# Performance work log

Measured on AMD Instinct MI355X. Metric: run time of the kernel, lower is better.

Reference implementation:

```python
import jax, jax.numpy as jnp
import numpy as np

B, N, D_SIM = 4096, 64, 768
NLI_DIM = 768
KK = 5
H1, NUM_CLASSES = 1024, 4


def setup_inputs() -> dict:
    key = jax.random.key(0)
    ks = jax.random.split(key, 8)
    sim_stance_emb = jax.random.normal(ks[0], (B, D_SIM), dtype=jnp.float32)
    nli_stance_emb = jax.random.normal(ks[1], (B, NLI_DIM), dtype=jnp.float32)
    sim_body_emb = jax.random.normal(ks[2], (B, N, D_SIM), dtype=jnp.float32)
    nli_body_emb = jax.random.normal(ks[3], (B, N, NLI_DIM), dtype=jnp.float32)
    fan1 = (KK + 1) * NLI_DIM
    W1 = jax.random.uniform(ks[4], (H1, fan1), jnp.float32, -1.0, 1.0) / jnp.sqrt(fan1)
    b1 = jax.random.uniform(ks[5], (H1,), jnp.float32, -1.0, 1.0) / jnp.sqrt(fan1)
    W2 = jax.random.uniform(ks[6], (NUM_CLASSES, H1), jnp.float32, -1.0, 1.0) / jnp.sqrt(H1)
    b2 = jax.random.uniform(ks[7], (NUM_CLASSES,), jnp.float32, -1.0, 1.0) / jnp.sqrt(H1)
    return {"sim_stance_emb": sim_stance_emb, "nli_stance_emb": nli_stance_emb,
            "sim_body_emb": sim_body_emb, "nli_body_emb": nli_body_emb,
            "W1": W1, "b1": b1, "W2": W2, "b2": b2}


def reference(sim_stance_emb, nli_stance_emb, sim_body_emb, nli_body_emb, W1, b1, W2, b2):
    # sims[b, n] = <sim_stance_emb[b], sim_body_emb[b, n]>  (bmm + squeeze)
    sims = jnp.einsum('bd,bnd->bn', sim_stance_emb, sim_body_emb)
    _, top_idx = jax.lax.top_k(sims, KK)                      # [B, KK]
    # gather top-k nli body sentence embeddings: [B, KK, NLI_DIM]
    top_emb = jnp.take_along_axis(nli_body_emb, top_idx[:, :, None], axis=1)
    xx = jnp.concatenate([nli_stance_emb, top_emb.reshape(top_emb.shape[0], -1)], axis=1)
    xx = jax.nn.relu(xx @ W1.T + b1)
    return xx @ W2.T + b2
```

## Files before the change

### kernel.cpp

```cpp
#include <hip/hip_runtime.h>
#include <stdint.h>
#include <stddef.h>

#define B_N   4096
#define NSENT 64
#define DDIM  768
#define TOPK  5
#define FAN1  4608
#define H1DIM 1024
#define NCLS  4
#define KDIM  4608
#define KHALF 2304

typedef __attribute__((ext_vector_type(8))) __bf16 bf16x8;
typedef __attribute__((ext_vector_type(4))) float  f32x4;

__device__ __forceinline__ unsigned short f2bf(float f) {
    unsigned int u = __float_as_uint(f);
    unsigned int r = (u + 0x7fffu + ((u >> 16) & 1u)) >> 16;
    return (unsigned short)r;
}

__device__ __forceinline__ void gl_lds16(const void* g, void* l) {
    __builtin_amdgcn_global_load_lds((__attribute__((address_space(1))) void*)(g),
                                     (__attribute__((address_space(3))) void*)(l),
                                     16, 0, 0);
}

__global__ __launch_bounds__(256) void k_topk_gather(
    const float* __restrict__ sim_stance,
    const float* __restrict__ sim_body,
    const float* __restrict__ nli_stance,
    const float* __restrict__ nli_body,
    unsigned short* __restrict__ xx)
{
    const int b    = blockIdx.x;
    const int tid  = threadIdx.x;
    const int lane = tid & 63;
    const int wave = tid >> 6;
    const int g    = lane >> 4;
    const int c    = lane & 15;
    __shared__ float sims[NSENT];
    __shared__ int   topidx[TOPK];

    const float4* st4 = (const float4*)(sim_stance + (size_t)b * DDIM);
    float4 st[12];
    #pragma unroll
    for (int j = 0; j < 12; ++j) st[j] = st4[c + 16 * j];

    const float* bodyb = sim_body + (size_t)b * NSENT * DDIM;
    #pragma unroll 1
    for (int it = 0; it < 4; ++it) {
        const int r = wave * 16 + it * 4 + g;
        const float4* r4 = (const float4*)(bodyb + (size_t)r * DDIM);
        float p = 0.f;
        #pragma unroll
        for (int j = 0; j < 12; ++j) {
            float4 v = r4[c + 16 * j];
            p += v.x*st[j].x + v.y*st[j].y + v.z*st[j].z + v.w*st[j].w;
        }
        #pragma unroll
        for (int off = 8; off; off >>= 1) p += __shfl_xor(p, off);
        if (c == 0) sims[r] = p;
    }
    __syncthreads();

    if (wave == 0) {
        float v = sims[lane];
        #pragma unroll
        for (int k = 0; k < TOPK; ++k) {
            float bv = v; int bi = lane;
            #pragma unroll
            for (int off = 32; off; off >>= 1) {
                float ov = __shfl_xor(bv, off);
                int   oi = __shfl_xor(bi, off);
                if (ov > bv || (ov == bv && oi < bi)) { bv = ov; bi = oi; }
            }
            if (lane == 0) topidx[k] = bi;
            if (lane == bi) v = -3.402823466e38f;
        }
    }
    __syncthreads();

    unsigned short* xrow = xx + (size_t)b * FAN1;
    for (int task = tid; task < 1152; task += 256) {
        const int seg = task / 192;
        const int t   = task - seg * 192;
        const float* src = (seg == 0)
            ? (nli_stance + (size_t)b * DDIM)
            : (nli_body + ((size_t)b * NSENT + topidx[seg - 1]) * DDIM);
        float4 v = ((const float4*)src)[t];
        ushort4 o;
        o.x = f2bf(v.x); o.y = f2bf(v.y); o.z = f2bf(v.z); o.w = f2bf(v.w);
        ((ushort4*)(xrow + seg * DDIM))[t] = o;
    }
}

__global__ __launch_bounds__(256) void k_f32_to_bf16x4(
    const float* __restrict__ in, unsigned short* __restrict__ o, int n4)
{
    int i = blockIdx.x * 256 + threadIdx.x;
    if (i < n4) {
        float4 v = ((const float4*)in)[i];
        ushort4 r;
        r.x = f2bf(v.x); r.y = f2bf(v.y); r.z = f2bf(v.z); r.w = f2bf(v.w);
        ((ushort4*)o)[i] = r;
    }
}

__global__ __launch_bounds__(256, 2) void k_gemm1(
    const unsigned short* __restrict__ A,
    const unsigned short* __restrict__ W,
    float* __restrict__ P)
{
    constexpr int BM = 128, BN = 128, BK = 64;
    constexpr int K = KDIM;
    __shared__ unsigned short lA[BM * BK];
    __shared__ unsigned short lB[BN * BK];

    const int tid = threadIdx.x, lane = tid & 63, wave = tid >> 6;
    const int bid = blockIdx.x;
    const int wk  = (bid & 7) * 64 + (bid >> 3);
    const int ks  = wk >> 8;
    const int rem = wk & 255;
    const int bm  = rem >> 3, bn = rem & 7;
    const int wm = wave >> 1, wn = wave & 1;
    const int k0 = ks * KHALF;

    const int rowq = wave * 8 + (lane >> 3);
    const int sc   = (lane & 7) ^ (lane >> 3);
    const unsigned short* gA[4];
    const unsigned short* gB[4];
    #pragma unroll
    for (int j = 0; j < 4; ++j) {
        gA[j] = A + (size_t)(bm * BM + j * 32 + rowq) * K + k0 + sc * 8;
        gB[j] = W + (size_t)(bn * BN + j * 32 + rowq) * K + k0 + sc * 8;
    }
    unsigned short* lAd[4];
    unsigned short* lBd[4];
    #pragma unroll
    for (int j = 0; j < 4; ++j) {
        lAd[j] = &lA[(j * 256 + wave * 64) * 8];
        lBd[j] = &lB[(j * 256 + wave * 64) * 8];
    }

    const int r16 = lane & 15;
    const int p0  = (lane >> 4) ^ (r16 & 7);
    const int p1  = p0 ^ 4;
    const unsigned short* paBase = &lA[(wm * 64 + r16) * BK];
    const unsigned short* pbBase = &lB[(wn * 64 + r16) * BK];

    f32x4 acc[4][4];
    #pragma unroll
    for (int m = 0; m < 4; ++m)
        #pragma unroll
        for (int n = 0; n < 4; ++n) acc[m][n] = {0.f, 0.f, 0.f, 0.f};

    for (int kt = 0; kt < KHALF / BK; ++kt) {
        #pragma unroll
        for (int j = 0; j < 4; ++j) { gl_lds16(gA[j], lAd[j]); gA[j] += BK; }
        #pragma unroll
        for (int j = 0; j < 4; ++j) { gl_lds16(gB[j], lBd[j]); gB[j] += BK; }
        __syncthreads();

        bf16x8 fa[4][2], fb[4][2];
        #pragma unroll
        for (int m = 0; m < 4; ++m) {
            fa[m][0] = *(const bf16x8*)(paBase + m * 16 * BK + p0 * 8);
            fa[m][1] = *(const bf16x8*)(paBase + m * 16 * BK + p1 * 8);
        }
        #pragma unroll
        for (int n = 0; n < 4; ++n) {
            fb[n][0] = *(const bf16x8*)(pbBase + n * 16 * BK + p0 * 8);
            fb[n][1] = *(const bf16x8*)(pbBase + n * 16 * BK + p1 * 8);
        }
        #pragma unroll
        for (int h = 0; h < 2; ++h)
            #pragma unroll
            for (int m = 0; m < 4; ++m)
                #pragma unroll
                for (int n = 0; n < 4; ++n)
                    acc[m][n] = __builtin_amdgcn_mfma_f32_16x16x32_bf16(
                        fa[m][h], fb[n][h], acc[m][n], 0, 0, 0);
        __syncthreads();
    }

    float* Pk = P + (size_t)ks * B_N * H1DIM;
    const int colbase = bn * BN + wn * 64 + r16;
    const int rowbase = bm * BM + wm * 64 + (lane >> 4) * 4;
    #pragma unroll
    for (int n = 0; n < 4; ++n) {
        const int col = colbase + n * 16;
        #pragma unroll
        for (int m = 0; m < 4; ++m) {
            const int row = rowbase + m * 16;
            #pragma unroll
            for (int j = 0; j < 4; ++j)
                Pk[(size_t)(row + j) * H1DIM + col] = acc[m][n][j];
        }
    }
}

__global__ __launch_bounds__(256) void k_gemm2(
    const float* __restrict__ P, const float* __restrict__ W2,
    const float* __restrict__ b1, const float* __restrict__ b2,
    float* __restrict__ out)
{
    __shared__ float w2s[NCLS * H1DIM + H1DIM];
    const int tid = threadIdx.x, lane = tid & 63, wave = tid >> 6;
    const int row = blockIdx.x * 4 + wave;
    for (int i = tid; i < NCLS * H1DIM; i += 256) w2s[i] = W2[i];
    for (int i = tid; i < H1DIM; i += 256) w2s[NCLS * H1DIM + i] = b1[i];
    __syncthreads();

    const float4* p0 = (const float4*)(P + (size_t)row * H1DIM);
    const float4* p1 = (const float4*)(P + (size_t)(B_N + row) * H1DIM);
    const float4* w0 = (const float4*)&w2s[0];
    const float4* w1 = (const float4*)&w2s[H1DIM];
    const float4* w2 = (const float4*)&w2s[2 * H1DIM];
    const float4* w3 = (const float4*)&w2s[3 * H1DIM];
    const float4* bb = (const float4*)&w2s[4 * H1DIM];
    float a0 = 0.f, a1 = 0.f, a2 = 0.f, a3 = 0.f;
    #pragma unroll
    for (int j = 0; j < 4; ++j) {
        const int idx = j * 64 + lane;
        float4 x0 = p0[idx], x1 = p1[idx], bv = bb[idx];
        float4 h;
        h.x = x0.x + x1.x + bv.x; h.x = h.x > 0.f ? h.x : 0.f;
        h.y = x0.y + x1.y + bv.y; h.y = h.y > 0.f ? h.y : 0.f;
        h.z = x0.z + x1.z + bv.z; h.z = h.z > 0.f ? h.z : 0.f;
        h.w = x0.w + x1.w + bv.w; h.w = h.w > 0.f ? h.w : 0.f;
        float4 xv;
        xv = w0[idx]; a0 += h.x*xv.x + h.y*xv.y + h.z*xv.z + h.w*xv.w;
        xv = w1[idx]; a1 += h.x*xv.x + h.y*xv.y + h.z*xv.z + h.w*xv.w;
        xv = w2[idx]; a2 += h.x*xv.x + h.y*xv.y + h.z*xv.z + h.w*xv.w;
        xv = w3[idx]; a3 += h.x*xv.x + h.y*xv.y + h.z*xv.z + h.w*xv.w;
    }
    #pragma unroll
    for (int off = 32; off; off >>= 1) {
        a0 += __shfl_xor(a0, off);
        a1 += __shfl_xor(a1, off);
        a2 += __shfl_xor(a2, off);
        a3 += __shfl_xor(a3, off);
    }
    if (lane == 0) {
        float* o = out + (size_t)row * NCLS;
        o[0] = a0 + b2[0]; o[1] = a1 + b2[1]; o[2] = a2 + b2[2]; o[3] = a3 + b2[3];
    }
}

extern "C" void kernel_launch(void* const* d_in, const int* in_sizes, int n_in,
                              void* d_out, int out_size, void* d_ws, size_t ws_size,
                              hipStream_t stream)
{
    const float* sim_stance = (const float*)d_in[0];
    const float* nli_stance = (const float*)d_in[1];
    const float* sim_body   = (const float*)d_in[2];
    const float* nli_body   = (const float*)d_in[3];
    const float* W1 = (const float*)d_in[4];
    const float* b1 = (const float*)d_in[5];
    const float* W2 = (const float*)d_in[6];
    const float* b2 = (const float*)d_in[7];
    float* out = (float*)d_out;

    char* ws = (char*)d_ws;
    unsigned short* xx  = (unsigned short*)ws;
    unsigned short* w1b = (unsigned short*)(ws + 37748736u);
    float*          P   = (float*)(ws + 37748736u + 9437184u);

    k_f32_to_bf16x4<<<dim3(4608), dim3(256), 0, stream>>>(W1, w1b, 1179648);
    k_topk_gather<<<dim3(B_N), dim3(256), 0, stream>>>(sim_stance, sim_body,
                                                       nli_stance, nli_body, xx);
    k_gemm1<<<dim3(512), dim3(256), 0, stream>>>(xx, w1b, P);
    k_gemm2<<<dim3(1024), dim3(256), 0, stream>>>(P, W2, b1, b2, out);
}
```

Baseline: 255.0 us.

## Double-buffer LDS tiles in split-K GEMM1 to overlap loads with MFMA

Splits the shared-memory A/B tiles into two buffers and software-pipelines the K loop, issuing the global-to-LDS copy for the next tile before computing on the current one. One barrier with vmcnt wait per step replaces the two syncthreads per tile. This is meant to hide global memory latency behind the MFMA work. LDS use per block doubles to 64KB, which may limit occupancy to fewer than the two blocks per CU the launch bounds request.

```diff
diff --git a/kernel.cpp b/kernel.cpp
--- a/kernel.cpp
+++ b/kernel.cpp
@@ -115,8 +115,9 @@
 {
     constexpr int BM = 128, BN = 128, BK = 64;
     constexpr int K = KDIM;
-    __shared__ unsigned short lA[BM * BK];
-    __shared__ unsigned short lB[BN * BK];
+    constexpr int NT = KHALF / BK;
+    __shared__ unsigned short lA[2][BM * BK];
+    __shared__ unsigned short lB[2][BN * BK];
 
     const int tid = threadIdx.x, lane = tid & 63, wave = tid >> 6;
     const int bid = blockIdx.x;
@@ -136,19 +137,13 @@
         gA[j] = A + (size_t)(bm * BM + j * 32 + rowq) * K + k0 + sc * 8;
         gB[j] = W + (size_t)(bn * BN + j * 32 + rowq) * K + k0 + sc * 8;
     }
-    unsigned short* lAd[4];
-    unsigned short* lBd[4];
-    #pragma unroll
-    for (int j = 0; j < 4; ++j) {
-        lAd[j] = &lA[(j * 256 + wave * 64) * 8];
-        lBd[j] = &lB[(j * 256 + wave * 64) * 8];
-    }
+    const int ldsOff = (wave * 64) * 8;
 
     const int r16 = lane & 15;
     const int p0  = (lane >> 4) ^ (r16 & 7);
     const int p1  = p0 ^ 4;
-    const unsigned short* paBase = &lA[(wm * 64 + r16) * BK];
-    const unsigned short* pbBase = &lB[(wn * 64 + r16) * BK];
+    const int aRowOff = (wm * 64 + r16) * BK;
+    const int bRowOff = (wn * 64 + r16) * BK;
 
     f32x4 acc[4][4];
     #pragma unroll
@@ -156,34 +151,53 @@
         #pragma unroll
         for (int n = 0; n < 4; ++n) acc[m][n] = {0.f, 0.f, 0.f, 0.f};
 
-    for (int kt = 0; kt < KHALF / BK; ++kt) {
-        #pragma unroll
-        for (int j = 0; j < 4; ++j) { gl_lds16(gA[j], lAd[j]); gA[j] += BK; }
-        #pragma unroll
-        for (int j = 0; j < 4; ++j) { gl_lds16(gB[j], lBd[j]); gB[j] += BK; }
-        __syncthreads();
-
-        bf16x8 fa[4][2], fb[4][2];
-        #pragma unroll
-        for (int m = 0; m < 4; ++m) {
-            fa[m][0] = *(const bf16x8*)(paBase + m * 16 * BK + p0 * 8);
-            fa[m][1] = *(const bf16x8*)(paBase + m * 16 * BK + p1 * 8);
-        }
-        #pragma unroll
-        for (int n = 0; n < 4; ++n) {
-            fb[n][0] = *(const bf16x8*)(pbBase + n * 16 * BK + p0 * 8);
-            fb[n][1] = *(const bf16x8*)(pbBase + n * 16 * BK + p1 * 8);
-        }
-        #pragma unroll
-        for (int h = 0; h < 2; ++h)
-            #pragma unroll
-            for (int m = 0; m < 4; ++m)
-                #pragma unroll
-                for (int n = 0; n < 4; ++n)
-                    acc[m][n] = __builtin_amdgcn_mfma_f32_16x16x32_bf16(
-                        fa[m][h], fb[n][h], acc[m][n], 0, 0, 0);
-        __syncthreads();
-    }
+#define STAGE(SEL, T) do {                                                  \
+    _Pragma("unroll")                                                       \
+    for (int j = 0; j < 4; ++j)                                             \
+        gl_lds16(gA[j] + (size_t)(T) * BK, &lA[SEL][j * 2048 + ldsOff]);    \
+    _Pragma("unroll")                                                       \
+    for (int j = 0; j < 4; ++j)                                             \
+        gl_lds16(gB[j] + (size_t)(T) * BK, &lB[SEL][j * 2048 + ldsOff]);    \
+} while (0)
+
+#define COMPUTE(SEL) do {                                                   \
+    bf16x8 fa[4][2], fb[4][2];                                              \
+    _Pragma("unroll")                                                       \
+    for (int m = 0; m < 4; ++m) {                                           \
+        fa[m][0] = *(const bf16x8*)(&lA[SEL][aRowOff + m * 16 * BK + p0 * 8]); \
+        fa[m][1] = *(const bf16x8*)(&lA[SEL][aRowOff + m * 16 * BK + p1 * 8]); \
+    }                                                                       \
+    _Pragma("unroll")                                                       \
+    for (int n = 0; n < 4; ++n) {                                           \
+        fb[n][0] = *(const bf16x8*)(&lB[SEL][bRowOff + n * 16 * BK + p0 * 8]); \
+        fb[n][1] = *(const bf16x8*)(&lB[SEL][bRowOff + n * 16 * BK + p1 * 8]); \
+    }                                                                       \
+    _Pragma("unroll")                                                       \
+    for (int h = 0; h < 2; ++h)                                             \
+        _Pragma("unroll")                                                   \
+        for (int m = 0; m < 4; ++m)                                         \
+            _Pragma("unroll")                                               \
+            for (int n = 0; n < 4; ++n)                                     \
+                acc[m][n] = __builtin_amdgcn_mfma_f32_16x16x32_bf16(        \
+                    fa[m][h], fb[n][h], acc[m][n], 0, 0, 0);                \
+} while (0)
+
+#define SYNCPIPE() asm volatile("s_waitcnt vmcnt(0)\n\ts_barrier" ::: "memory")
+
+    STAGE(0, 0);
+    SYNCPIPE();
+    #pragma unroll 1
+    for (int it = 0; it < 17; ++it) {
+        const int t = 2 * it;
+        STAGE(1, t + 1); COMPUTE(0); SYNCPIPE();
+        STAGE(0, t + 2); COMPUTE(1); SYNCPIPE();
+    }
+    STAGE(1, 35); COMPUTE(0); SYNCPIPE();
+    COMPUTE(1);
+
+#undef STAGE
+#undef COMPUTE
+#undef SYNCPIPE
 
     float* Pk = P + (size_t)ks * B_N * H1DIM;
     const int colbase = bn * BN + wn * 64 + r16;
```

New measurement: 257.3 us. About the same (+0.9%).
